# Performance work log

Hardware: AMD Instinct MI355X
Metric: run time of the kernel (lower is better)

## Reference

```python
import jax, jax.numpy as jnp
import numpy as np

# Constants from mode='only_tv': gamma_l1=gamma_dwt=beta=lambda_l1=lambda_dwt=sigma=0,
# so u_l1,u_dwt,z,eta_l1,eta_dwt,rho stay identically zero and drop out of the math.
GAMMA_TV = 2.0
ALPHA = 5.0
LAMBDA_TV = 1e-4
N_ITER = 200


def soft_thresh(v, t):
    return jnp.sign(v) * jnp.maximum(jnp.abs(v) - t, 0.0)


def setup_inputs() -> dict:
    key = jax.random.key(0)
    k1, k2, k3 = jax.random.split(key, 3)
    target = jax.random.normal(k1, (4096, 64), dtype=jnp.float32)  # B spectra of K bands
    A = jax.random.normal(k2, (9, 64), dtype=jnp.float32) * 0.1     # (M=9 channels, K=64 bands)
    x0 = jax.random.normal(k3, (4096, 64), dtype=jnp.float32)       # replaces randn_like(target)
    return {"target": target, "A": A, "x0": x0}


def reference(target, A, x0):
    # target, x0: (B, K) batch of per-sample length-K vectors; A: (M, K)
    K = A.shape[1]
    AT = A.T  # (K, M)
    I = jnp.eye(K, dtype=A.dtype)
    Delta = jnp.roll(I, 1, axis=1) - I          # (K, K)
    DtD = Delta.T @ Delta
    inv_item = jnp.linalg.inv(AT @ A + GAMMA_TV * DtD + ALPHA * I)  # (K, K)

    # b = A @ x  per sample  ->  (B, M);  AT @ b per sample -> (B, K)
    b = target @ A.T
    ATb = b @ A

    # per-sample Delta @ v, batched over rows -> v_mat @ Delta.T
    def D(v):
        return v @ Delta.T

    eta_tv0 = jnp.zeros_like(x0)
    tau0 = jnp.zeros_like(x0)

    def step(carry, _):
        x, eta_tv, tau = carry
        u_tv = soft_thresh(D(x) + eta_tv / GAMMA_TV, LAMBDA_TV / GAMMA_TV)
        w = jnp.maximum(x + tau / ALPHA, 0.0)
        # note: torch's matmul(z_tv, DeltaT) on a vector equals Delta @ z_tv -> batched D(.)
        resid = ATb + D(GAMMA_TV * u_tv - eta_tv) + ALPHA * w - tau
        x = resid @ inv_item.T  # per-sample inv_item @ resid
        eta_tv = eta_tv + GAMMA_TV * (D(x) - u_tv)
        tau = tau + ALPHA * (x - w)
        return (x, eta_tv, tau), None

    (x, _, _), _ = jax.lax.scan(step, (x0, eta_tv0, tau0), None, length=N_ITER)
    return x
```

## Files before the change

kernel.cpp:

```cpp
#include <hip/hip_runtime.h>

#define NSAMP 4096
#define NITER 200

__global__ __launch_bounds__(256) void setup_woodbury(const float* __restrict__ A,
                                                      float* __restrict__ inv_out) {
  __shared__ double lamr[64];
  __shared__ float binv[64];
  __shared__ float P[9][64];
  __shared__ float Q[9][64];
  __shared__ double W[9][18];
  const int tid = threadIdx.x;
  const double TWO_PI = 6.283185307179586476925286766559;

  double cb = 0.0;
  if (tid < 64) {
    cb = cos(TWO_PI * (double)tid / 64.0);
    lamr[tid] = 1.0 / (9.0 - 4.0 * cb);
  }
  __syncthreads();
  if (tid < 64) {
    double cm1 = 1.0, c0 = cb;
    double acc = lamr[0] + cb * lamr[1];
#pragma unroll 16
    for (int m = 2; m < 64; ++m) {
      double c = 2.0 * cb * c0 - cm1;
      cm1 = c0;
      c0 = c;
      acc += c * lamr[m];
    }
    binv[tid] = (float)(acc / 64.0);
  }
  __syncthreads();

  for (int e = tid; e < 9 * 64; e += 256) {
    int m = e >> 6, i = e & 63;
    double acc = 0.0;
#pragma unroll 16
    for (int k = 0; k < 64; ++k)
      acc += (double)A[m * 64 + k] * (double)binv[(k - i) & 63];
    P[m][i] = (float)acc;
  }
  __syncthreads();

  if (tid < 81) {
    int m = tid / 9, n = tid % 9;
    double acc = (m == n) ? 1.0 : 0.0;
#pragma unroll 16
    for (int i = 0; i < 64; ++i)
      acc += (double)P[m][i] * (double)A[n * 64 + i];
    W[m][n] = acc;
    W[m][n + 9] = (m == n) ? 1.0 : 0.0;
  }
  __syncthreads();

  {
    const int r9 = tid / 18, c9 = tid % 18;
    const bool act = (tid < 162);
    for (int k = 0; k < 9; ++k) {
      double pv = 1.0, f = 0.0, wkc = 0.0;
      if (act) {
        pv = W[k][k];
        f = W[r9][k];
        wkc = W[k][c9];
      }
      __syncthreads();
      if (act) {
        double nk = wkc / pv;
        W[r9][c9] = (r9 == k) ? nk : fma(-f, nk, W[r9][c9]);
      }
      __syncthreads();
    }
  }

  for (int e = tid; e < 9 * 64; e += 256) {
    int m = e >> 6, j = e & 63;
    double acc = 0.0;
#pragma unroll
    for (int n = 0; n < 9; ++n) acc += W[m][n + 9] * (double)P[n][j];
    Q[m][j] = (float)acc;
  }
  __syncthreads();

  for (int e = tid; e < 64 * 64; e += 256) {
    int i = e >> 6, j = e & 63;
    float acc = binv[(i - j) & 63];
#pragma unroll
    for (int m = 0; m < 9; ++m) acc = fmaf(-P[m][i], Q[m][j], acc);
    inv_out[e] = acc;
  }
}

__global__ __launch_bounds__(256)
void admm_kernel(const float* __restrict__ target, const float* __restrict__ A,
                 const float* __restrict__ x0, const float* __restrict__ invmat,
                 float* __restrict__ out) {
  __shared__ __align__(16) float rbuf[4][64];
  const int tid = threadIdx.x;
  const int wid = tid >> 6;
  const int lane = tid & 63;
  const int s = blockIdx.x * 4 + wid;

  float t = target[s * 64 + lane];
  float atbv = 0.f;
#pragma unroll
  for (int m = 0; m < 9; ++m) {
    float a = A[m * 64 + lane];
    float p = t * a;
#pragma unroll
    for (int off = 32; off; off >>= 1) p += __shfl_xor(p, off, 64);
    atbv = fmaf(a, p, atbv);
  }

  const float* mrow = invmat + (size_t)lane * 64;
  unsigned int rb_base = (unsigned int)(uintptr_t)(&rbuf[wid][0]);
  unsigned int a_w = rb_base + lane * 4;
  unsigned int a_nxt = ((lane + 1) & 63) * 4;
  float xin = x0[s * 64 + lane];
  float xout;
  int cnt_s;
  const int smask = 0x7fffffff;
  const float sthr = 5e-5f, sc02 = 0.2f, sc5 = 5.0f;

  asm volatile(
      "s_mov_b32 m0, -1\n\t"
      "global_load_dwordx4 v[64:67],   %[mp], off\n\t"
      "global_load_dwordx4 v[68:71],   %[mp], off offset:16\n\t"
      "global_load_dwordx4 v[72:75],   %[mp], off offset:32\n\t"
      "global_load_dwordx4 v[76:79],   %[mp], off offset:48\n\t"
      "global_load_dwordx4 v[80:83],   %[mp], off offset:64\n\t"
      "global_load_dwordx4 v[84:87],   %[mp], off offset:80\n\t"
      "global_load_dwordx4 v[88:91],   %[mp], off offset:96\n\t"
      "global_load_dwordx4 v[92:95],   %[mp], off offset:112\n\t"
      "global_load_dwordx4 v[96:99],   %[mp], off offset:128\n\t"
      "global_load_dwordx4 v[100:103], %[mp], off offset:144\n\t"
      "global_load_dwordx4 v[104:107], %[mp], off offset:160\n\t"
      "global_load_dwordx4 v[108:111], %[mp], off offset:176\n\t"
      "global_load_dwordx4 v[112:115], %[mp], off offset:192\n\t"
      "global_load_dwordx4 v[116:119], %[mp], off offset:208\n\t"
      "global_load_dwordx4 v[120:123], %[mp], off offset:224\n\t"
      "global_load_dwordx4 v[124:127], %[mp], off offset:240\n\t"
      "v_mov_b32 v32, %[xin]\n\t"
      "v_mov_b32 v36, %[atb]\n\t"
      "v_mov_b32 v33, 0\n\t"
      "v_mov_b32 v34, 0\n\t"
      "ds_bpermute_b32 v45, %[anx], v32\n\t"
      "s_waitcnt lgkmcnt(0)\n\t"
      "v_sub_f32 v35, v45, v32\n\t"
      "s_movk_i32 %[cnt], 200\n\t"
      "s_waitcnt vmcnt(0)\n\t"
      "1:\n\t"
      "v_fma_f32 v40, 0.5, v33, v35\n\t"
      "v_and_b32 v41, %[msk], v40\n\t"
      "v_subrev_f32 v41, %[thr], v41\n\t"
      "v_max_f32 v41, 0, v41\n\t"
      "v_bfi_b32 v42, %[msk], v41, v40\n\t"
      "v_fma_f32 v43, %[c02], v34, v32\n\t"
      "v_max_f32 v43, 0, v43\n\t"
      "v_fma_f32 v40, 2.0, v42, -v33\n\t"
      "ds_bpermute_b32 v45, %[anx], v40\n\t"
      "v_fma_f32 v44, %[c5], v43, v36\n\t"
      "v_sub_f32 v44, v44, v34\n\t"
      "v_sub_f32 v44, v44, v40\n\t"
      "s_waitcnt lgkmcnt(0)\n\t"
      "v_add_f32 v44, v44, v45\n\t"
      "ds_write_b32 %[aw], v44\n\t"
      "ds_read_b128 v[48:51], %[rb]\n\t"
      "ds_read_b128 v[52:55], %[rb] offset:16\n\t"
      "ds_read_b128 v[56:59], %[rb] offset:32\n\t"
      "ds_read_b128 v[60:63], %[rb] offset:48\n\t"
      "s_waitcnt lgkmcnt(3)\n\t"
      "v_pk_mul_f32 v[44:45], v[64:65], v[48:49]\n\t"
      "v_pk_mul_f32 v[46:47], v[66:67], v[50:51]\n\t"
      "ds_read_b128 v[48:51], %[rb] offset:64\n\t"
      "s_waitcnt lgkmcnt(3)\n\t"
      "v_pk_fma_f32 v[44:45], v[68:69], v[52:53], v[44:45]\n\t"
      "v_pk_fma_f32 v[46:47], v[70:71], v[54:55], v[46:47]\n\t"
      "ds_read_b128 v[52:55], %[rb] offset:80\n\t"
      "s_waitcnt lgkmcnt(3)\n\t"
      "v_pk_fma_f32 v[44:45], v[72:73], v[56:57], v[44:45]\n\t"
      "v_pk_fma_f32 v[46:47], v[74:75], v[58:59], v[46:47]\n\t"
      "ds_read_b128 v[56:59], %[rb] offset:96\n\t"
      "s_waitcnt lgkmcnt(3)\n\t"
      "v_pk_fma_f32 v[44:45], v[76:77], v[60:61], v[44:45]\n\t"
      "v_pk_fma_f32 v[46:47], v[78:79], v[62:63], v[46:47]\n\t"
      "ds_read_b128 v[60:63], %[rb] offset:112\n\t"
      "s_waitcnt lgkmcnt(3)\n\t"
      "v_pk_fma_f32 v[44:45], v[80:81], v[48:49], v[44:45]\n\t"
      "v_pk_fma_f32 v[46:47], v[82:83], v[50:51], v[46:47]\n\t"
      "ds_read_b128 v[48:51], %[rb] offset:128\n\t"
      "s_waitcnt lgkmcnt(3)\n\t"
      "v_pk_fma_f32 v[44:45], v[84:85], v[52:53], v[44:45]\n\t"
      "v_pk_fma_f32 v[46:47], v[86:87], v[54:55], v[46:47]\n\t"
      "ds_read_b128 v[52:55], %[rb] offset:144\n\t"
      "s_waitcnt lgkmcnt(3)\n\t"
      "v_pk_fma_f32 v[44:45], v[88:89], v[56:57], v[44:45]\n\t"
      "v_pk_fma_f32 v[46:47], v[90:91], v[58:59], v[46:47]\n\t"
      "ds_read_b128 v[56:59], %[rb] offset:160\n\t"
      "s_waitcnt lgkmcnt(3)\n\t"
      "v_pk_fma_f32 v[44:45], v[92:93], v[60:61], v[44:45]\n\t"
      "v_pk_fma_f32 v[46:47], v[94:95], v[62:63], v[46:47]\n\t"
      "ds_read_b128 v[60:63], %[rb] offset:176\n\t"
      "s_waitcnt lgkmcnt(3)\n\t"
      "v_pk_fma_f32 v[44:45], v[96:97], v[48:49], v[44:45]\n\t"
      "v_pk_fma_f32 v[46:47], v[98:99], v[50:51], v[46:47]\n\t"
      "ds_read_b128 v[48:51], %[rb] offset:192\n\t"
      "s_waitcnt lgkmcnt(3)\n\t"
      "v_pk_fma_f32 v[44:45], v[100:101], v[52:53], v[44:45]\n\t"
      "v_pk_fma_f32 v[46:47], v[102:103], v[54:55], v[46:47]\n\t"
      "ds_read_b128 v[52:55], %[rb] offset:208\n\t"
      "s_waitcnt lgkmcnt(3)\n\t"
      "v_pk_fma_f32 v[44:45], v[104:105], v[56:57], v[44:45]\n\t"
      "v_pk_fma_f32 v[46:47], v[106:107], v[58:59], v[46:47]\n\t"
      "ds_read_b128 v[56:59], %[rb] offset:224\n\t"
      "s_waitcnt lgkmcnt(3)\n\t"
      "v_pk_fma_f32 v[44:45], v[108:109], v[60:61], v[44:45]\n\t"
      "v_pk_fma_f32 v[46:47], v[110:111], v[62:63], v[46:47]\n\t"
      "ds_read_b128 v[60:63], %[rb] offset:240\n\t"
      "s_waitcnt lgkmcnt(3)\n\t"
      "v_pk_fma_f32 v[44:45], v[112:113], v[48:49], v[44:45]\n\t"
      "v_pk_fma_f32 v[46:47], v[114:115], v[50:51], v[46:47]\n\t"
      "s_waitcnt lgkmcnt(2)\n\t"
      "v_pk_fma_f32 v[44:45], v[116:117], v[52:53], v[44:45]\n\t"
      "v_pk_fma_f32 v[46:47], v[118:119], v[54:55], v[46:47]\n\t"
      "s_waitcnt lgkmcnt(1)\n\t"
      "v_pk_fma_f32 v[44:45], v[120:121], v[56:57], v[44:45]\n\t"
      "v_pk_fma_f32 v[46:47], v[122:123], v[58:59], v[46:47]\n\t"
      "s_waitcnt lgkmcnt(0)\n\t"
      "v_pk_fma_f32 v[44:45], v[124:125], v[60:61], v[44:45]\n\t"
      "v_pk_fma_f32 v[46:47], v[126:127], v[62:63], v[46:47]\n\t"
      "v_pk_add_f32 v[44:45], v[44:45], v[46:47]\n\t"
      "v_add_f32 v32, v44, v45\n\t"
      "ds_bpermute_b32 v45, %[anx], v32\n\t"
      "s_waitcnt lgkmcnt(0)\n\t"
      "v_sub_f32 v35, v45, v32\n\t"
      "v_sub_f32 v41, v35, v42\n\t"
      "v_fma_f32 v33, 2.0, v41, v33\n\t"
      "v_sub_f32 v41, v32, v43\n\t"
      "v_fma_f32 v34, %[c5], v41, v34\n\t"
      "s_sub_u32 %[cnt], %[cnt], 1\n\t"
      "s_cmp_lg_u32 %[cnt], 0\n\t"
      "s_cbranch_scc1 1b\n\t"
      "v_mov_b32 %[xout], v32\n\t"
      : [xout] "=v"(xout), [cnt] "=&s"(cnt_s)
      : [mp] "v"(mrow), [rb] "v"(rb_base), [aw] "v"(a_w), [anx] "v"(a_nxt),
        [xin] "v"(xin), [atb] "v"(atbv),
        [msk] "s"(smask), [thr] "s"(sthr), [c02] "s"(sc02), [c5] "s"(sc5)
      : "memory", "scc",
        "v32","v33","v34","v35","v36","v37","v38","v39","v40","v41","v42","v43",
        "v44","v45","v46","v47","v48","v49","v50","v51","v52","v53","v54","v55",
        "v56","v57","v58","v59","v60","v61","v62","v63","v64","v65","v66","v67",
        "v68","v69","v70","v71","v72","v73","v74","v75","v76","v77","v78","v79",
        "v80","v81","v82","v83","v84","v85","v86","v87","v88","v89","v90","v91",
        "v92","v93","v94","v95","v96","v97","v98","v99","v100","v101","v102",
        "v103","v104","v105","v106","v107","v108","v109","v110","v111","v112",
        "v113","v114","v115","v116","v117","v118","v119","v120","v121","v122",
        "v123","v124","v125","v126","v127");

  out[s * 64 + lane] = xout;
}

extern "C" void kernel_launch(void* const* d_in, const int* in_sizes, int n_in,
                              void* d_out, int out_size, void* d_ws, size_t ws_size,
                              hipStream_t stream) {
  const float* target = (const float*)d_in[0];
  const float* A = (const float*)d_in[1];
  const float* x0 = (const float*)d_in[2];
  float* out = (float*)d_out;
  float* inv_ws = (float*)d_ws;

  setup_woodbury<<<1, 256, 0, stream>>>(A, inv_ws);
  admm_kernel<<<NSAMP / 4, 256, 0, stream>>>(target, A, x0, inv_ws, out);
}
```

Measured before the change: 202.6 us.

## Replace LDS broadcast matvec with DPP row-rotate FMAs and pre-permuted matrix

The per-iteration 64x64 matvec no longer writes the residual to LDS and reads it back as broadcast vectors. Each lane now gathers other lanes' residuals through DPP row_ror modifiers fused into v_fmac, plus a few swizzle/bpermute steps to cross 16-lane rows. The setup kernel stores the inverse matrix with columns permuted to match that rotation order, and detects the DPP rotate direction at runtime. This removes the LDS round trip and its waits from the loop. In exchange it adds DPP hazard nops and loses the packed FMA throughput.

```diff
diff --git a/kernel.cpp b/kernel.cpp
--- a/kernel.cpp
+++ b/kernel.cpp
@@ -4,12 +4,13 @@
 #define NITER 200
 
 __global__ __launch_bounds__(256) void setup_woodbury(const float* __restrict__ A,
-                                                      float* __restrict__ inv_out) {
+                                                      float* __restrict__ mperm) {
   __shared__ double lamr[64];
   __shared__ float binv[64];
   __shared__ float P[9][64];
   __shared__ float Q[9][64];
   __shared__ double W[9][18];
+  __shared__ float Mfull[64][64];
   const int tid = threadIdx.x;
   const double TWO_PI = 6.283185307179586476925286766559;
 
@@ -87,15 +88,39 @@
     float acc = binv[(i - j) & 63];
 #pragma unroll
     for (int m = 0; m < 9; ++m) acc = fmaf(-P[m][i], Q[m][j], acc);
-    inv_out[e] = acc;
+    Mfull[i][j] = acc;
+  }
+  __syncthreads();
+
+  if (tid < 64) {
+    const int lid = tid;
+    int dpp1;
+    asm volatile(
+        "s_nop 4\n\t"
+        "v_mov_b32_dpp %0, %1 row_ror:1 row_mask:0xf bank_mask:0xf\n\t"
+        "s_nop 4"
+        : "=v"(dpp1)
+        : "v"(lid));
+    const int lane0val = __builtin_amdgcn_readfirstlane(dpp1);
+    const int dir = (lane0val == 1) ? 1 : -1;
+    const int xs4[4] = {0, 16, 48, 32};
+    for (int s = 0; s < 4; ++s) {
+      for (int t = 0; t < 16; ++t) {
+        int q = (lid & 48) | (((lid & 15) + dir * t + 16) & 15);
+        int j = q ^ xs4[s];
+        mperm[lid * 64 + 16 * s + t] = Mfull[lid][j];
+      }
+    }
   }
 }
+
+#define DPL(op, acc, rr, mm, rot) \
+  op " " acc ", " rr ", " mm " row_ror:" #rot " row_mask:0xf bank_mask:0xf\n\t"
 
 __global__ __launch_bounds__(256)
 void admm_kernel(const float* __restrict__ target, const float* __restrict__ A,
-                 const float* __restrict__ x0, const float* __restrict__ invmat,
+                 const float* __restrict__ x0, const float* __restrict__ mperm,
                  float* __restrict__ out) {
-  __shared__ __align__(16) float rbuf[4][64];
   const int tid = threadIdx.x;
   const int wid = tid >> 6;
   const int lane = tid & 63;
@@ -112,10 +137,9 @@
     atbv = fmaf(a, p, atbv);
   }
 
-  const float* mrow = invmat + (size_t)lane * 64;
-  unsigned int rb_base = (unsigned int)(uintptr_t)(&rbuf[wid][0]);
-  unsigned int a_w = rb_base + lane * 4;
+  const float* mrow = mperm + (size_t)lane * 64;
   unsigned int a_nxt = ((lane + 1) & 63) * 4;
+  unsigned int a_x32 = (lane ^ 32) * 4;
   float xin = x0[s * 64 + lane];
   float xout;
   int cnt_s;
@@ -164,92 +188,100 @@
       "v_sub_f32 v44, v44, v40\n\t"
       "s_waitcnt lgkmcnt(0)\n\t"
       "v_add_f32 v44, v44, v45\n\t"
-      "ds_write_b32 %[aw], v44\n\t"
-      "ds_read_b128 v[48:51], %[rb]\n\t"
-      "ds_read_b128 v[52:55], %[rb] offset:16\n\t"
-      "ds_read_b128 v[56:59], %[rb] offset:32\n\t"
-      "ds_read_b128 v[60:63], %[rb] offset:48\n\t"
-      "s_waitcnt lgkmcnt(3)\n\t"
-      "v_pk_mul_f32 v[44:45], v[64:65], v[48:49]\n\t"
-      "v_pk_mul_f32 v[46:47], v[66:67], v[50:51]\n\t"
-      "ds_read_b128 v[48:51], %[rb] offset:64\n\t"
-      "s_waitcnt lgkmcnt(3)\n\t"
-      "v_pk_fma_f32 v[44:45], v[68:69], v[52:53], v[44:45]\n\t"
-      "v_pk_fma_f32 v[46:47], v[70:71], v[54:55], v[46:47]\n\t"
-      "ds_read_b128 v[52:55], %[rb] offset:80\n\t"
-      "s_waitcnt lgkmcnt(3)\n\t"
-      "v_pk_fma_f32 v[44:45], v[72:73], v[56:57], v[44:45]\n\t"
-      "v_pk_fma_f32 v[46:47], v[74:75], v[58:59], v[46:47]\n\t"
-      "ds_read_b128 v[56:59], %[rb] offset:96\n\t"
-      "s_waitcnt lgkmcnt(3)\n\t"
-      "v_pk_fma_f32 v[44:45], v[76:77], v[60:61], v[44:45]\n\t"
-      "v_pk_fma_f32 v[46:47], v[78:79], v[62:63], v[46:47]\n\t"
-      "ds_read_b128 v[60:63], %[rb] offset:112\n\t"
-      "s_waitcnt lgkmcnt(3)\n\t"
-      "v_pk_fma_f32 v[44:45], v[80:81], v[48:49], v[44:45]\n\t"
-      "v_pk_fma_f32 v[46:47], v[82:83], v[50:51], v[46:47]\n\t"
-      "ds_read_b128 v[48:51], %[rb] offset:128\n\t"
-      "s_waitcnt lgkmcnt(3)\n\t"
-      "v_pk_fma_f32 v[44:45], v[84:85], v[52:53], v[44:45]\n\t"
-      "v_pk_fma_f32 v[46:47], v[86:87], v[54:55], v[46:47]\n\t"
-      "ds_read_b128 v[52:55], %[rb] offset:144\n\t"
-      "s_waitcnt lgkmcnt(3)\n\t"
-      "v_pk_fma_f32 v[44:45], v[88:89], v[56:57], v[44:45]\n\t"
-      "v_pk_fma_f32 v[46:47], v[90:91], v[58:59], v[46:47]\n\t"
-      "ds_read_b128 v[56:59], %[rb] offset:160\n\t"
-      "s_waitcnt lgkmcnt(3)\n\t"
-      "v_pk_fma_f32 v[44:45], v[92:93], v[60:61], v[44:45]\n\t"
-      "v_pk_fma_f32 v[46:47], v[94:95], v[62:63], v[46:47]\n\t"
-      "ds_read_b128 v[60:63], %[rb] offset:176\n\t"
-      "s_waitcnt lgkmcnt(3)\n\t"
-      "v_pk_fma_f32 v[44:45], v[96:97], v[48:49], v[44:45]\n\t"
-      "v_pk_fma_f32 v[46:47], v[98:99], v[50:51], v[46:47]\n\t"
-      "ds_read_b128 v[48:51], %[rb] offset:192\n\t"
-      "s_waitcnt lgkmcnt(3)\n\t"
-      "v_pk_fma_f32 v[44:45], v[100:101], v[52:53], v[44:45]\n\t"
-      "v_pk_fma_f32 v[46:47], v[102:103], v[54:55], v[46:47]\n\t"
-      "ds_read_b128 v[52:55], %[rb] offset:208\n\t"
-      "s_waitcnt lgkmcnt(3)\n\t"
-      "v_pk_fma_f32 v[44:45], v[104:105], v[56:57], v[44:45]\n\t"
-      "v_pk_fma_f32 v[46:47], v[106:107], v[58:59], v[46:47]\n\t"
-      "ds_read_b128 v[56:59], %[rb] offset:224\n\t"
-      "s_waitcnt lgkmcnt(3)\n\t"
-      "v_pk_fma_f32 v[44:45], v[108:109], v[60:61], v[44:45]\n\t"
-      "v_pk_fma_f32 v[46:47], v[110:111], v[62:63], v[46:47]\n\t"
-      "ds_read_b128 v[60:63], %[rb] offset:240\n\t"
-      "s_waitcnt lgkmcnt(3)\n\t"
-      "v_pk_fma_f32 v[44:45], v[112:113], v[48:49], v[44:45]\n\t"
-      "v_pk_fma_f32 v[46:47], v[114:115], v[50:51], v[46:47]\n\t"
-      "s_waitcnt lgkmcnt(2)\n\t"
-      "v_pk_fma_f32 v[44:45], v[116:117], v[52:53], v[44:45]\n\t"
-      "v_pk_fma_f32 v[46:47], v[118:119], v[54:55], v[46:47]\n\t"
-      "s_waitcnt lgkmcnt(1)\n\t"
-      "v_pk_fma_f32 v[44:45], v[120:121], v[56:57], v[44:45]\n\t"
-      "v_pk_fma_f32 v[46:47], v[122:123], v[58:59], v[46:47]\n\t"
-      "s_waitcnt lgkmcnt(0)\n\t"
-      "v_pk_fma_f32 v[44:45], v[124:125], v[60:61], v[44:45]\n\t"
-      "v_pk_fma_f32 v[46:47], v[126:127], v[62:63], v[46:47]\n\t"
-      "v_pk_add_f32 v[44:45], v[44:45], v[46:47]\n\t"
-      "v_add_f32 v32, v44, v45\n\t"
+      "ds_swizzle_b32 v47, v44 offset:0x401F\n\t"
+      "v_mul_f32 v37, v44, v64\n\t"
+      DPL("v_mul_f32",  "v38", "v44", "v65", 1)
+      DPL("v_mul_f32",  "v39", "v44", "v66", 2)
+      DPL("v_mul_f32",  "v46", "v44", "v67", 3)
+      DPL("v_fmac_f32", "v37", "v44", "v68", 4)
+      DPL("v_fmac_f32", "v38", "v44", "v69", 5)
+      DPL("v_fmac_f32", "v39", "v44", "v70", 6)
+      DPL("v_fmac_f32", "v46", "v44", "v71", 7)
+      DPL("v_fmac_f32", "v37", "v44", "v72", 8)
+      DPL("v_fmac_f32", "v38", "v44", "v73", 9)
+      DPL("v_fmac_f32", "v39", "v44", "v74", 10)
+      DPL("v_fmac_f32", "v46", "v44", "v75", 11)
+      DPL("v_fmac_f32", "v37", "v44", "v76", 12)
+      DPL("v_fmac_f32", "v38", "v44", "v77", 13)
+      DPL("v_fmac_f32", "v39", "v44", "v78", 14)
+      DPL("v_fmac_f32", "v46", "v44", "v79", 15)
+      "s_waitcnt lgkmcnt(0)\n\t"
+      "ds_bpermute_b32 v48, %[a32], v47\n\t"
+      "s_nop 1\n\t"
+      "v_fmac_f32 v37, v47, v80\n\t"
+      DPL("v_fmac_f32", "v38", "v47", "v81", 1)
+      DPL("v_fmac_f32", "v39", "v47", "v82", 2)
+      DPL("v_fmac_f32", "v46", "v47", "v83", 3)
+      DPL("v_fmac_f32", "v37", "v47", "v84", 4)
+      DPL("v_fmac_f32", "v38", "v47", "v85", 5)
+      DPL("v_fmac_f32", "v39", "v47", "v86", 6)
+      DPL("v_fmac_f32", "v46", "v47", "v87", 7)
+      DPL("v_fmac_f32", "v37", "v47", "v88", 8)
+      DPL("v_fmac_f32", "v38", "v47", "v89", 9)
+      DPL("v_fmac_f32", "v39", "v47", "v90", 10)
+      DPL("v_fmac_f32", "v46", "v47", "v91", 11)
+      DPL("v_fmac_f32", "v37", "v47", "v92", 12)
+      DPL("v_fmac_f32", "v38", "v47", "v93", 13)
+      DPL("v_fmac_f32", "v39", "v47", "v94", 14)
+      DPL("v_fmac_f32", "v46", "v47", "v95", 15)
+      "s_waitcnt lgkmcnt(0)\n\t"
+      "ds_swizzle_b32 v49, v48 offset:0x401F\n\t"
+      "s_nop 1\n\t"
+      "v_fmac_f32 v37, v48, v96\n\t"
+      DPL("v_fmac_f32", "v38", "v48", "v97", 1)
+      DPL("v_fmac_f32", "v39", "v48", "v98", 2)
+      DPL("v_fmac_f32", "v46", "v48", "v99", 3)
+      DPL("v_fmac_f32", "v37", "v48", "v100", 4)
+      DPL("v_fmac_f32", "v38", "v48", "v101", 5)
+      DPL("v_fmac_f32", "v39", "v48", "v102", 6)
+      DPL("v_fmac_f32", "v46", "v48", "v103", 7)
+      DPL("v_fmac_f32", "v37", "v48", "v104", 8)
+      DPL("v_fmac_f32", "v38", "v48", "v105", 9)
+      DPL("v_fmac_f32", "v39", "v48", "v106", 10)
+      DPL("v_fmac_f32", "v46", "v48", "v107", 11)
+      DPL("v_fmac_f32", "v37", "v48", "v108", 12)
+      DPL("v_fmac_f32", "v38", "v48", "v109", 13)
+      DPL("v_fmac_f32", "v39", "v48", "v110", 14)
+      DPL("v_fmac_f32", "v46", "v48", "v111", 15)
+      "s_waitcnt lgkmcnt(0)\n\t"
+      "s_nop 1\n\t"
+      "v_fmac_f32 v37, v49, v112\n\t"
+      DPL("v_fmac_f32", "v38", "v49", "v113", 1)
+      DPL("v_fmac_f32", "v39", "v49", "v114", 2)
+      DPL("v_fmac_f32", "v46", "v49", "v115", 3)
+      DPL("v_fmac_f32", "v37", "v49", "v116", 4)
+      DPL("v_fmac_f32", "v38", "v49", "v117", 5)
+      DPL("v_fmac_f32", "v39", "v49", "v118", 6)
+      DPL("v_fmac_f32", "v46", "v49", "v119", 7)
+      DPL("v_fmac_f32", "v37", "v49", "v120", 8)
+      DPL("v_fmac_f32", "v38", "v49", "v121", 9)
+      DPL("v_fmac_f32", "v39", "v49", "v122", 10)
+      DPL("v_fmac_f32", "v46", "v49", "v123", 11)
+      DPL("v_fmac_f32", "v37", "v49", "v124", 12)
+      DPL("v_fmac_f32", "v38", "v49", "v125", 13)
+      DPL("v_fmac_f32", "v39", "v49", "v126", 14)
+      DPL("v_fmac_f32", "v46", "v49", "v127", 15)
+      "v_add_f32 v37, v37, v38\n\t"
+      "v_add_f32 v39, v39, v46\n\t"
+      "v_add_f32 v32, v37, v39\n\t"
       "ds_bpermute_b32 v45, %[anx], v32\n\t"
+      "v_sub_f32 v41, v32, v43\n\t"
+      "v_fma_f32 v34, %[c5], v41, v34\n\t"
       "s_waitcnt lgkmcnt(0)\n\t"
       "v_sub_f32 v35, v45, v32\n\t"
       "v_sub_f32 v41, v35, v42\n\t"
       "v_fma_f32 v33, 2.0, v41, v33\n\t"
-      "v_sub_f32 v41, v32, v43\n\t"
-      "v_fma_f32 v34, %[c5], v41, v34\n\t"
       "s_sub_u32 %[cnt], %[cnt], 1\n\t"
       "s_cmp_lg_u32 %[cnt], 0\n\t"
       "s_cbranch_scc1 1b\n\t"
       "v_mov_b32 %[xout], v32\n\t"
       : [xout] "=v"(xout), [cnt] "=&s"(cnt_s)
-      : [mp] "v"(mrow), [rb] "v"(rb_base), [aw] "v"(a_w), [anx] "v"(a_nxt),
+      : [mp] "v"(mrow), [anx] "v"(a_nxt), [a32] "v"(a_x32),
         [xin] "v"(xin), [atb] "v"(atbv),
         [msk] "s"(smask), [thr] "s"(sthr), [c02] "s"(sc02), [c5] "s"(sc5)
       : "memory", "scc",
         "v32","v33","v34","v35","v36","v37","v38","v39","v40","v41","v42","v43",
-        "v44","v45","v46","v47","v48","v49","v50","v51","v52","v53","v54","v55",
-        "v56","v57","v58","v59","v60","v61","v62","v63","v64","v65","v66","v67",
+        "v44","v45","v46","v47","v48","v49","v64","v65","v66","v67",
         "v68","v69","v70","v71","v72","v73","v74","v75","v76","v77","v78","v79",
         "v80","v81","v82","v83","v84","v85","v86","v87","v88","v89","v90","v91",
         "v92","v93","v94","v95","v96","v97","v98","v99","v100","v101","v102",
@@ -267,8 +299,8 @@
   const float* A = (const float*)d_in[1];
   const float* x0 = (const float*)d_in[2];
   float* out = (float*)d_out;
-  float* inv_ws = (float*)d_ws;
-
-  setup_woodbury<<<1, 256, 0, stream>>>(A, inv_ws);
-  admm_kernel<<<NSAMP / 4, 256, 0, stream>>>(target, A, x0, inv_ws, out);
+  float* mperm = (float*)d_ws;
+
+  setup_woodbury<<<1, 256, 0, stream>>>(A, mperm);
+  admm_kernel<<<NSAMP / 4, 256, 0, stream>>>(target, A, x0, mperm, out);
 }
```

New measurement: 201.1 us. About the same (-0.8%).
